# Kernel tuning notes

Measured on AMD Instinct MI355X. Metric: run time of the kernel, lower is better.

Reference implementation:

```python
import jax, jax.numpy as jnp
import numpy as np

N_NODES = 100000


def _gcn_norm(edge_index, n):
    # PyG GCNConv: add self-loops, symmetric normalization D^-1/2 (A+I) D^-1/2
    loops = jnp.arange(n, dtype=edge_index.dtype)
    src = jnp.concatenate([edge_index[0], loops])
    dst = jnp.concatenate([edge_index[1], loops])
    deg = jax.ops.segment_sum(jnp.ones_like(dst, dtype=jnp.float32), dst, num_segments=n)
    dis = jnp.where(deg > 0, jax.lax.rsqrt(jnp.maximum(deg, 1.0)), 0.0)
    norm = dis[src] * dis[dst]  # [E + n]
    return src, dst, norm


def _gcn_layer(h, W, b, src, dst, norm, n):
    h = h @ W                              # dense projection [n, out]
    msg = h[src] * norm[:, None]           # gather + scale   [E+n, out]
    agg = jax.ops.segment_sum(msg, dst, num_segments=n)  # scatter-add
    return agg + b


def setup_inputs() -> dict:
    key = jax.random.key(0)
    ks = jax.random.split(key, 8)
    n, f, h, d, e = N_NODES, 256, 128, 64, 1600000
    x = jax.random.normal(ks[0], (n, f), dtype=jnp.float32)
    edge_index = jax.random.randint(ks[1], (2, e), 0, n, dtype=jnp.int64)
    s1 = 1.0 / np.sqrt(f)
    s2 = 1.0 / np.sqrt(h)
    return {
        "x": x,
        "edge_index": edge_index,
        "W1": jax.random.normal(ks[2], (f, h), dtype=jnp.float32) * s1,
        "b1": jnp.zeros((h,), dtype=jnp.float32),
        "Wmu": jax.random.normal(ks[3], (h, d), dtype=jnp.float32) * s2,
        "bmu": jnp.zeros((d,), dtype=jnp.float32),
        "Wvar": jax.random.normal(ks[4], (h, d), dtype=jnp.float32) * s2,
        "bvar": jnp.zeros((d,), dtype=jnp.float32),
    }


def reference(x, edge_index, W1, b1, Wmu, bmu, Wvar, bvar):
    n = x.shape[0]
    src, dst, norm = _gcn_norm(edge_index, n)
    h = jax.nn.relu(_gcn_layer(x, W1, b1, src, dst, norm, n))
    mu = _gcn_layer(h, Wmu, bmu, src, dst, norm, n)
    sigma = _gcn_layer(h, Wvar, bvar, src, dst, norm, n)
    return mu, sigma
```

## Files before the change

kernel.cpp:

```cpp
#include <hip/hip_runtime.h>


#define HID 128
#define DOUT 64
#define NB_SHIFT 8
#define CHUNK 8192
#define MAXNB 400

typedef _Float16 half_t;
typedef half_t f16x4 __attribute__((ext_vector_type(4)));
typedef half_t f16x8 __attribute__((ext_vector_type(8)));
typedef float  f32x4 __attribute__((ext_vector_type(4)));


__global__ __launch_bounds__(256) void bincount_kernel(const int* __restrict__ dst,
                                                       int* __restrict__ counts,
                                                       int E, int nblocks, int NB) {
    __shared__ int hist[MAXNB];
    const int b = blockIdx.x;
    for (int t = threadIdx.x; t < NB; t += 256) hist[t] = 0;
    __syncthreads();
    const int beg = b * CHUNK;
    const int end = min(E, beg + CHUNK);
    for (int e = beg + threadIdx.x; e < end; e += 256)
        atomicAdd(&hist[dst[e] >> NB_SHIFT], 1);
    __syncthreads();
    for (int t = threadIdx.x; t < NB; t += 256)
        counts[t * nblocks + b] = hist[t];
}

__global__ __launch_bounds__(256) void scan1_kernel(const int* __restrict__ in,
                                                    int* __restrict__ out,
                                                    int* __restrict__ bsum, int n) {
    __shared__ int s[256];
    int b = blockIdx.x, t = threadIdx.x;
    int base = b * 1024 + t * 4;
    int v0 = 0, v1 = 0, v2 = 0, v3 = 0;
    if (base + 0 < n) v0 = in[base + 0];
    if (base + 1 < n) v1 = in[base + 1];
    if (base + 2 < n) v2 = in[base + 2];
    if (base + 3 < n) v3 = in[base + 3];
    int tsum = v0 + v1 + v2 + v3;
    s[t] = tsum;
    __syncthreads();
    for (int off = 1; off < 256; off <<= 1) {
        int x = (t >= off) ? s[t - off] : 0;
        __syncthreads();
        s[t] += x;
        __syncthreads();
    }
    int excl = s[t] - tsum;
    if (base + 0 < n) out[base + 0] = excl;
    if (base + 1 < n) out[base + 1] = excl + v0;
    if (base + 2 < n) out[base + 2] = excl + v0 + v1;
    if (base + 3 < n) out[base + 3] = excl + v0 + v1 + v2;
    if (t == 255) bsum[b] = s[255];
}

__global__ __launch_bounds__(1024) void scan2_kernel(int* __restrict__ bsum, int nb) {
    __shared__ int s[1024];
    int t = threadIdx.x;
    int v = (t < nb) ? bsum[t] : 0;
    s[t] = v;
    __syncthreads();
    for (int off = 1; off < 1024; off <<= 1) {
        int x = (t >= off) ? s[t - off] : 0;
        __syncthreads();
        s[t] += x;
        __syncthreads();
    }
    if (t < nb) bsum[t] = s[t] - v;
}

__global__ void scan3_kernel(int* __restrict__ out, const int* __restrict__ bsum, int n) {
    int i = blockIdx.x * blockDim.x + threadIdx.x;
    if (i < n) out[i] += bsum[i >> 10];
}

__global__ __launch_bounds__(1024) void binscatter_kernel(const int* __restrict__ src,
                                                          const int* __restrict__ dst,
                                                          const int* __restrict__ offsets,
                                                          int2* __restrict__ binned,
                                                          int E, int nblocks, int NB) {
    __shared__ int  lhist[1024];
    __shared__ int  lbase[1024];
    __shared__ int  cur[1024];
    __shared__ int  goff[MAXNB];
    __shared__ int2 staged[CHUNK];
    const int b = blockIdx.x, t = threadIdx.x;
    const int beg = b * CHUNK;
    const int end = min(E, beg + CHUNK);
    const int ne  = end - beg;

    lhist[t] = 0;
    for (int k = t; k < NB; k += 1024) goff[k] = offsets[k * nblocks + b];
    __syncthreads();

    int2 regs[8];
    #pragma unroll
    for (int j = 0; j < 8; j++) {
        int e = beg + t + j * 1024;
        if (e < end) {
            regs[j] = make_int2(src[e], dst[e]);
            atomicAdd(&lhist[regs[j].y >> NB_SHIFT], 1);
        }
    }
    __syncthreads();

    int hv = lhist[t];
    for (int off = 1; off < 1024; off <<= 1) {
        int x = (t >= off) ? lhist[t - off] : 0;
        __syncthreads();
        lhist[t] += x;
        __syncthreads();
    }
    lbase[t] = lhist[t] - hv;
    cur[t]   = lhist[t] - hv;
    __syncthreads();

    #pragma unroll
    for (int j = 0; j < 8; j++) {
        int e = beg + t + j * 1024;
        if (e < end) {
            int pos = atomicAdd(&cur[regs[j].y >> NB_SHIFT], 1);
            staged[pos] = regs[j];
        }
    }
    __syncthreads();

    #pragma unroll
    for (int j = 0; j < 8; j++) {
        int tt = t + j * 1024;
        if (tt < ne) {
            int2 sd = staged[tt];
            int bkt = sd.y >> NB_SHIFT;
            binned[goff[bkt] + (tt - lbase[bkt])] = sd;
        }
    }
}

__global__ __launch_bounds__(256) void csrbuild_kernel(const int2* __restrict__ binned,
                                                       const int* __restrict__ offsets,
                                                       int* __restrict__ rowptr_end,
                                                       int* __restrict__ colA,
                                                       float* __restrict__ dis,
                                                       int E, int nblocks, int NB, int n) {
    __shared__ int deg[256];
    __shared__ int sc[256];
    __shared__ int cur[256];
    const int b = blockIdx.x;
    const int t = threadIdx.x;
    const int base = offsets[b * nblocks];
    const int bend = (b + 1 < NB) ? offsets[(b + 1) * nblocks] : E;

    deg[t] = 0;
    __syncthreads();
    for (int e = base + t; e < bend; e += 256)
        atomicAdd(&deg[binned[e].y & 255], 1);
    __syncthreads();

    int v = deg[t];
    sc[t] = v;
    __syncthreads();
    for (int off = 1; off < 256; off <<= 1) {
        int x = (t >= off) ? sc[t - off] : 0;
        __syncthreads();
        sc[t] += x;
        __syncthreads();
    }
    int incl = sc[t];
    int node = (b << NB_SHIFT) + t;
    if (node < n) {
        rowptr_end[node] = base + incl;
        dis[node] = rsqrtf((float)v + 1.0f);
    }
    cur[t] = base + incl - v;
    __syncthreads();

    for (int e = base + t; e < bend; e += 256) {
        int2 sd = binned[e];
        int pos = atomicAdd(&cur[sd.y & 255], 1);
        colA[pos] = sd.x;
    }
}

__global__ void w1t_kernel(const float* __restrict__ W1, half_t* __restrict__ W1T) {
    int i = blockIdx.x * blockDim.x + threadIdx.x;
    int k = i >> 7, nn = i & 127;
    W1T[nn * 256 + k] = (half_t)W1[i];
}
__global__ void wcatt_kernel(const float* __restrict__ Wmu, const float* __restrict__ Wvar,
                             half_t* __restrict__ WcatT) {
    int i = blockIdx.x * blockDim.x + threadIdx.x;
    int k = i >> 7, nn = i & 127;
    float v = (nn < DOUT) ? Wmu[k * DOUT + nn] : Wvar[k * DOUT + (nn - DOUT)];
    WcatT[nn * 128 + k] = (half_t)v;
}

__global__ __launch_bounds__(256) void gemm1_mfma(const float* __restrict__ A,
                                                  const half_t* __restrict__ BT,
                                                  const float* __restrict__ dis,
                                                  half_t* __restrict__ C, int M) {
    __shared__ half_t As[64][72];
    __shared__ half_t Bs[128][72];
    const int tid = threadIdx.x;
    const int block_row = blockIdx.x * 64;
    const int wave = tid >> 6, lane = tid & 63;
    const int wm = (wave & 1) * 32, wn = (wave >> 1) * 64;
    const int l16 = lane & 15, quad = lane >> 4;

    f32x4 acc[2][4] = {};
    float4 pa[4];
    f16x8  pb[4];

    #pragma unroll
    for (int i = 0; i < 4; i++) {
        int idx = tid + i * 256;
        int r = idx >> 4, c = idx & 15;
        int row = block_row + r; row = row < M ? row : M - 1;
        pa[i] = ((const float4*)(A + (size_t)row * 256))[c];
    }
    #pragma unroll
    for (int i = 0; i < 4; i++) {
        int idx = tid + i * 256;
        int nr = idx >> 3, kc = idx & 7;
        pb[i] = *(const f16x8*)(BT + (size_t)nr * 256 + kc * 8);
    }

    for (int k0 = 0; k0 < 256; k0 += 64) {
        #pragma unroll
        for (int i = 0; i < 4; i++) {
            int idx = tid + i * 256;
            int r = idx >> 4, c = idx & 15;
            f16x4 hv = { (half_t)pa[i].x, (half_t)pa[i].y, (half_t)pa[i].z, (half_t)pa[i].w };
            *(f16x4*)(&As[r][c * 4]) = hv;
        }
        #pragma unroll
        for (int i = 0; i < 4; i++) {
            int idx = tid + i * 256;
            int nr = idx >> 3, kc = idx & 7;
            *(f16x8*)(&Bs[nr][kc * 8]) = pb[i];
        }
        __syncthreads();

        if (k0 < 192) {
            #pragma unroll
            for (int i = 0; i < 4; i++) {
                int idx = tid + i * 256;
                int r = idx >> 4, c = idx & 15;
                int row = block_row + r; row = row < M ? row : M - 1;
                pa[i] = ((const float4*)(A + (size_t)row * 256 + k0 + 64))[c];
            }
            #pragma unroll
            for (int i = 0; i < 4; i++) {
                int idx = tid + i * 256;
                int nr = idx >> 3, kc = idx & 7;
                pb[i] = *(const f16x8*)(BT + (size_t)nr * 256 + k0 + 64 + kc * 8);
            }
        }

        #pragma unroll
        for (int ks = 0; ks < 2; ks++) {
            f16x8 af[2], bf[4];
            #pragma unroll
            for (int mt = 0; mt < 2; mt++)
                af[mt] = *(const f16x8*)(&As[wm + mt * 16 + l16][ks * 32 + quad * 8]);
            #pragma unroll
            for (int nt = 0; nt < 4; nt++)
                bf[nt] = *(const f16x8*)(&Bs[wn + nt * 16 + l16][ks * 32 + quad * 8]);
            #pragma unroll
            for (int mt = 0; mt < 2; mt++)
                #pragma unroll
                for (int nt = 0; nt < 4; nt++)
                    acc[mt][nt] = __builtin_amdgcn_mfma_f32_16x16x32_f16(af[mt], bf[nt], acc[mt][nt], 0, 0, 0);
        }
        __syncthreads();
    }

    #pragma unroll
    for (int mt = 0; mt < 2; mt++) {
        #pragma unroll
        for (int r = 0; r < 4; r++) {
            int row = block_row + wm + mt * 16 + quad * 4 + r;
            if (row < M) {
                float d = dis[row];
                #pragma unroll
                for (int nt = 0; nt < 4; nt++) {
                    int col = wn + nt * 16 + l16;
                    C[(size_t)row * 128 + col] = (half_t)(acc[mt][nt][r] * d);
                }
            }
        }
    }
}

__global__ __launch_bounds__(256) void gemm2_mfma(const half_t* __restrict__ A,
                                                  const half_t* __restrict__ BT,
                                                  const float* __restrict__ bmu,
                                                  const float* __restrict__ bvar,
                                                  float* __restrict__ out_mu,
                                                  float* __restrict__ out_sig, int M) {
    __shared__ half_t As[64][72];
    __shared__ half_t Bs[128][72];
    const int tid = threadIdx.x;
    const int block_row = blockIdx.x * 64;
    const int wave = tid >> 6, lane = tid & 63;
    const int wm = (wave & 1) * 32, wn = (wave >> 1) * 64;
    const int l16 = lane & 15, quad = lane >> 4;

    f32x4 acc[2][4] = {};
    f16x8 pa[2], pb[4];

    #pragma unroll
    for (int i = 0; i < 2; i++) {
        int idx = tid + i * 256;
        int r = idx >> 3, kc = idx & 7;
        int row = block_row + r; row = row < M ? row : M - 1;
        pa[i] = *(const f16x8*)(A + (size_t)row * 128 + kc * 8);
    }
    #pragma unroll
    for (int i = 0; i < 4; i++) {
        int idx = tid + i * 256;
        int nr = idx >> 3, kc = idx & 7;
        pb[i] = *(const f16x8*)(BT + (size_t)nr * 128 + kc * 8);
    }

    for (int k0 = 0; k0 < 128; k0 += 64) {
        #pragma unroll
        for (int i = 0; i < 2; i++) {
            int idx = tid + i * 256;
            int r = idx >> 3, kc = idx & 7;
            *(f16x8*)(&As[r][kc * 8]) = pa[i];
        }
        #pragma unroll
        for (int i = 0; i < 4; i++) {
            int idx = tid + i * 256;
            int nr = idx >> 3, kc = idx & 7;
            *(f16x8*)(&Bs[nr][kc * 8]) = pb[i];
        }
        __syncthreads();

        if (k0 < 64) {
            #pragma unroll
            for (int i = 0; i < 2; i++) {
                int idx = tid + i * 256;
                int r = idx >> 3, kc = idx & 7;
                int row = block_row + r; row = row < M ? row : M - 1;
                pa[i] = *(const f16x8*)(A + (size_t)row * 128 + 64 + kc * 8);
            }
            #pragma unroll
            for (int i = 0; i < 4; i++) {
                int idx = tid + i * 256;
                int nr = idx >> 3, kc = idx & 7;
                pb[i] = *(const f16x8*)(BT + (size_t)nr * 128 + 64 + kc * 8);
            }
        }

        #pragma unroll
        for (int ks = 0; ks < 2; ks++) {
            f16x8 af[2], bf[4];
            #pragma unroll
            for (int mt = 0; mt < 2; mt++)
                af[mt] = *(const f16x8*)(&As[wm + mt * 16 + l16][ks * 32 + quad * 8]);
            #pragma unroll
            for (int nt = 0; nt < 4; nt++)
                bf[nt] = *(const f16x8*)(&Bs[wn + nt * 16 + l16][ks * 32 + quad * 8]);
            #pragma unroll
            for (int mt = 0; mt < 2; mt++)
                #pragma unroll
                for (int nt = 0; nt < 4; nt++)
                    acc[mt][nt] = __builtin_amdgcn_mfma_f32_16x16x32_f16(af[mt], bf[nt], acc[mt][nt], 0, 0, 0);
        }
        __syncthreads();
    }

    float bias[4];
    int cols[4];
    #pragma unroll
    for (int nt = 0; nt < 4; nt++) {
        int col = wn + nt * 16 + l16;
        cols[nt] = col;
        bias[nt] = (col < DOUT) ? bmu[col] : bvar[col - DOUT];
    }

    #pragma unroll
    for (int mt = 0; mt < 2; mt++) {
        #pragma unroll
        for (int r = 0; r < 4; r++) {
            int row = block_row + wm + mt * 16 + quad * 4 + r;
            if (row < M) {
                #pragma unroll
                for (int nt = 0; nt < 4; nt++) {
                    int col = cols[nt];
                    float v = acc[mt][nt][r] + bias[nt];
                    if (col < DOUT) out_mu[(size_t)row * DOUT + col] = v;
                    else            out_sig[(size_t)row * DOUT + (col - DOUT)] = v;
                }
            }
        }
    }
}

__device__ __forceinline__ void acc_mix(float& a0, float& a1, float& a2, float& a3,
                                        f16x4 v, float fl) {
    union { f16x4 h; int i[2]; } u; u.h = v;
    asm("v_fma_mix_f32 %0, %1, %2, %0 op_sel_hi:[1,0,0]"
        : "+v"(a0) : "v"(u.i[0]), "v"(fl));
    asm("v_fma_mix_f32 %0, %1, %2, %0 op_sel:[1,0,0] op_sel_hi:[1,0,0]"
        : "+v"(a1) : "v"(u.i[0]), "v"(fl));
    asm("v_fma_mix_f32 %0, %1, %2, %0 op_sel_hi:[1,0,0]"
        : "+v"(a2) : "v"(u.i[1]), "v"(fl));
    asm("v_fma_mix_f32 %0, %1, %2, %0 op_sel:[1,0,0] op_sel_hi:[1,0,0]"
        : "+v"(a3) : "v"(u.i[1]), "v"(fl));
}

template <bool LAYER1>
__global__ __launch_bounds__(256) void agg_kernel(const int* __restrict__ rowptr_end,
                                                  const int* __restrict__ col,
                                                  const float* __restrict__ dis,
                                                  const half_t* __restrict__ hin,
                                                  half_t* __restrict__ hout,
                                                  const float* __restrict__ bias, int n) {
    int node = blockIdx.x * 8 + (threadIdx.x >> 5);
    if (node >= n) return;
    int lane = threadIdx.x & 31;
    int beg = (node == 0) ? 0 : rowptr_end[node - 1];
    int end = rowptr_end[node];
    const f16x4* hv = (const f16x4*)hin;

    float one = 1.0f;
    float ax = 0.f, ay = 0.f, az = 0.f, aw = 0.f;
    acc_mix(ax, ay, az, aw, hv[(size_t)node * 32 + lane], one);

    int deg = end - beg;
    if (deg > 0) {
        const int last = end - 1;
        int c[8];
        #pragma unroll
        for (int j = 0; j < 8; j++) c[j] = col[min(beg + j, last)];

        int ng = (deg + 7) >> 3;
        int e = beg;
        for (int g = 0; g < ng; g++) {
            f16x4 v[8];
            #pragma unroll
            for (int j = 0; j < 8; j++) v[j] = hv[(size_t)c[j] * 32 + lane];

            int enext = e + 8;
            if (g + 1 < ng) {
                #pragma unroll
                for (int j = 0; j < 8; j++) c[j] = col[min(enext + j, last)];
                #pragma unroll
                for (int j = 0; j < 8; j++) acc_mix(ax, ay, az, aw, v[j], one);
            } else {
                int rem = end - e;
                #pragma unroll
                for (int j = 0; j < 8; j++) {
                    float fl = (j < rem) ? 1.0f : 0.0f;
                    acc_mix(ax, ay, az, aw, v[j], fl);
                }
            }
            e = enext;
        }
    }

    float di = dis[node];
    if (LAYER1) {
        const float4 b = ((const float4*)bias)[lane];
        ax = ax * di + b.x; ay = ay * di + b.y; az = az * di + b.z; aw = aw * di + b.w;
        ax = (ax > 0.f ? ax : 0.f) * di;
        ay = (ay > 0.f ? ay : 0.f) * di;
        az = (az > 0.f ? az : 0.f) * di;
        aw = (aw > 0.f ? aw : 0.f) * di;
    } else {
        ax *= di; ay *= di; az *= di; aw *= di;
    }
    f16x4 o = { (half_t)ax, (half_t)ay, (half_t)az, (half_t)aw };
    ((f16x4*)hout)[(size_t)node * 32 + lane] = o;
}

extern "C" void kernel_launch(void* const* d_in, const int* in_sizes, int n_in,
                              void* d_out, int out_size, void* d_ws, size_t ws_size,
                              hipStream_t stream) {
    const float* x    = (const float*)d_in[0];
    const int*   ei   = (const int*)d_in[1];
    const float* W1   = (const float*)d_in[2];
    const float* b1   = (const float*)d_in[3];
    const float* Wmu  = (const float*)d_in[4];
    const float* bmu  = (const float*)d_in[5];
    const float* Wvar = (const float*)d_in[6];
    const float* bvar = (const float*)d_in[7];

    const int n = in_sizes[0] / 256;
    const int E = in_sizes[1] / 2;
    const int* src = ei;
    const int* dst = ei + E;

    const int NB      = (n + 255) >> NB_SHIFT;
    const int nblocks = (E + CHUNK - 1) / CHUNK;
    const int flat    = NB * nblocks;
    const int nb_scan = (flat + 1023) / 1024;

    char* ws = (char*)d_ws;
    size_t off = 0;
    auto alloc = [&](size_t bytes) { void* p = ws + off; off = (off + bytes + 255) & ~(size_t)255; return p; };
    float*  dis     = (float*) alloc((size_t)n * 4);
    int*    rowptr  = (int*)   alloc((size_t)n * 4);
    int*    counts  = (int*)   alloc((size_t)flat * 4);
    int*    offsets = (int*)   alloc((size_t)flat * 4);
    int*    bsum    = (int*)   alloc((size_t)nb_scan * 4 + 256);
    int2*   binned  = (int2*)  alloc((size_t)E * 8);
    int*    col     = (int*)   alloc((size_t)E * 4);
    half_t* W1T     = (half_t*)alloc((size_t)256 * HID * 2);
    half_t* WcatT   = (half_t*)alloc((size_t)HID * HID * 2);
    half_t* hs      = (half_t*)alloc((size_t)n * HID * 2);
    half_t* h1s     = (half_t*)alloc((size_t)n * HID * 2);
    half_t* agg2    = hs;

    float* out_mu  = (float*)d_out;
    float* out_sig = (float*)d_out + (size_t)n * DOUT;

    bincount_kernel<<<nblocks, 256, 0, stream>>>(dst, counts, E, nblocks, NB);
    scan1_kernel<<<nb_scan, 256, 0, stream>>>(counts, offsets, bsum, flat);
    scan2_kernel<<<1, 1024, 0, stream>>>(bsum, nb_scan);
    scan3_kernel<<<(flat + 255) / 256, 256, 0, stream>>>(offsets, bsum, flat);
    binscatter_kernel<<<nblocks, 1024, 0, stream>>>(src, dst, offsets, binned, E, nblocks, NB);
    csrbuild_kernel<<<NB, 256, 0, stream>>>(binned, offsets, rowptr, col, dis, E, nblocks, NB, n);

    w1t_kernel<<<(256 * HID) / 256, 256, 0, stream>>>(W1, W1T);
    wcatt_kernel<<<(HID * HID) / 256, 256, 0, stream>>>(Wmu, Wvar, WcatT);

    gemm1_mfma<<<(n + 63) / 64, 256, 0, stream>>>(x, W1T, dis, hs, n);
    agg_kernel<true><<<(n + 7) / 8, 256, 0, stream>>>(rowptr, col, dis, hs, h1s, b1, n);
    agg_kernel<false><<<(n + 7) / 8, 256, 0, stream>>>(rowptr, col, dis, h1s, agg2, nullptr, n);
    gemm2_mfma<<<(n + 63) / 64, 256, 0, stream>>>(agg2, WcatT, bmu, bvar, out_mu, out_sig, n);
}
```

Baseline: 217.6 us.

## Store hidden features in column-chunked layout and split aggregation by feature chunk

The hidden feature matrices now use a chunk-major layout of 8 chunks of 16 halves per node, written by gemm1 and read by gemm2 and the aggregation kernels. The aggregation grid is multiplied by 8 so each block handles one feature chunk, with 8 edge slots per node processed in parallel and reduced through warp shuffles. The aim is to make each chunk's working set (n×16 halves) fit in cache, so the random neighbour gathers hit cache more often. In exchange, the col array is read 8 times over, shuffle reductions are added, and each gather is only 8 bytes wide.

```diff
diff --git a/kernel.cpp b/kernel.cpp
--- a/kernel.cpp
+++ b/kernel.cpp
@@ -286,8 +286,8 @@
                 float d = dis[row];
                 #pragma unroll
                 for (int nt = 0; nt < 4; nt++) {
-                    int col = wn + nt * 16 + l16;
-                    C[(size_t)row * 128 + col] = (half_t)(acc[mt][nt][r] * d);
+                    int cchunk = (wn >> 4) + nt;
+                    C[((size_t)cchunk * M + row) * 16 + l16] = (half_t)(acc[mt][nt][r] * d);
                 }
             }
         }
@@ -316,7 +316,7 @@
         int idx = tid + i * 256;
         int r = idx >> 3, kc = idx & 7;
         int row = block_row + r; row = row < M ? row : M - 1;
-        pa[i] = *(const f16x8*)(A + (size_t)row * 128 + kc * 8);
+        pa[i] = *(const f16x8*)(A + ((size_t)(kc >> 1) * M + row) * 16 + (kc & 1) * 8);
     }
     #pragma unroll
     for (int i = 0; i < 4; i++) {
@@ -346,7 +346,7 @@
                 int idx = tid + i * 256;
                 int r = idx >> 3, kc = idx & 7;
                 int row = block_row + r; row = row < M ? row : M - 1;
-                pa[i] = *(const f16x8*)(A + (size_t)row * 128 + 64 + kc * 8);
+                pa[i] = *(const f16x8*)(A + ((size_t)(4 + (kc >> 1)) * M + row) * 16 + (kc & 1) * 8);
             }
             #pragma unroll
             for (int i = 0; i < 4; i++) {
@@ -421,62 +421,63 @@
                                                   const half_t* __restrict__ hin,
                                                   half_t* __restrict__ hout,
                                                   const float* __restrict__ bias, int n) {
-    int node = blockIdx.x * 8 + (threadIdx.x >> 5);
+    const int chunk = blockIdx.x & 7;
+    const int node  = (blockIdx.x >> 3) * 8 + (threadIdx.x >> 5);
     if (node >= n) return;
-    int lane = threadIdx.x & 31;
-    int beg = (node == 0) ? 0 : rowptr_end[node - 1];
-    int end = rowptr_end[node];
-    const f16x4* hv = (const f16x4*)hin;
-
-    float one = 1.0f;
+    const int lane32 = threadIdx.x & 31;
+    const int fq   = lane32 & 3;
+    const int slot = lane32 >> 2;
+
+    const f16x4* hc = (const f16x4*)(hin + (size_t)chunk * n * 16);
+
+    int beg = (node == 0) ? 0 : __builtin_nontemporal_load(&rowptr_end[node - 1]);
+    int end = __builtin_nontemporal_load(&rowptr_end[node]);
+
     float ax = 0.f, ay = 0.f, az = 0.f, aw = 0.f;
-    acc_mix(ax, ay, az, aw, hv[(size_t)node * 32 + lane], one);
+    {
+        f16x4 sv = hc[node * 4 + fq];
+        float fl = (slot == 0) ? 1.0f : 0.0f;
+        acc_mix(ax, ay, az, aw, sv, fl);
+    }
 
     int deg = end - beg;
     if (deg > 0) {
         const int last = end - 1;
-        int c[8];
-        #pragma unroll
-        for (int j = 0; j < 8; j++) c[j] = col[min(beg + j, last)];
-
+        int e = beg + slot;
+        int c = __builtin_nontemporal_load(&col[min(e, last)]);
         int ng = (deg + 7) >> 3;
-        int e = beg;
         for (int g = 0; g < ng; g++) {
-            f16x4 v[8];
-            #pragma unroll
-            for (int j = 0; j < 8; j++) v[j] = hv[(size_t)c[j] * 32 + lane];
-
-            int enext = e + 8;
-            if (g + 1 < ng) {
-                #pragma unroll
-                for (int j = 0; j < 8; j++) c[j] = col[min(enext + j, last)];
-                #pragma unroll
-                for (int j = 0; j < 8; j++) acc_mix(ax, ay, az, aw, v[j], one);
-            } else {
-                int rem = end - e;
-                #pragma unroll
-                for (int j = 0; j < 8; j++) {
-                    float fl = (j < rem) ? 1.0f : 0.0f;
-                    acc_mix(ax, ay, az, aw, v[j], fl);
-                }
-            }
-            e = enext;
-        }
-    }
-
-    float di = dis[node];
-    if (LAYER1) {
-        const float4 b = ((const float4*)bias)[lane];
-        ax = ax * di + b.x; ay = ay * di + b.y; az = az * di + b.z; aw = aw * di + b.w;
-        ax = (ax > 0.f ? ax : 0.f) * di;
-        ay = (ay > 0.f ? ay : 0.f) * di;
-        az = (az > 0.f ? az : 0.f) * di;
-        aw = (aw > 0.f ? aw : 0.f) * di;
-    } else {
-        ax *= di; ay *= di; az *= di; aw *= di;
-    }
-    f16x4 o = { (half_t)ax, (half_t)ay, (half_t)az, (half_t)aw };
-    ((f16x4*)hout)[(size_t)node * 32 + lane] = o;
+            f16x4 v = hc[c * 4 + fq];
+            int en = e + 8;
+            c = __builtin_nontemporal_load(&col[min(en, last)]);
+            float fl = (e <= last) ? 1.0f : 0.0f;
+            acc_mix(ax, ay, az, aw, v, fl);
+            e = en;
+        }
+    }
+
+    ax += __shfl_xor(ax, 4);  ay += __shfl_xor(ay, 4);
+    az += __shfl_xor(az, 4);  aw += __shfl_xor(aw, 4);
+    ax += __shfl_xor(ax, 8);  ay += __shfl_xor(ay, 8);
+    az += __shfl_xor(az, 8);  aw += __shfl_xor(aw, 8);
+    ax += __shfl_xor(ax, 16); ay += __shfl_xor(ay, 16);
+    az += __shfl_xor(az, 16); aw += __shfl_xor(aw, 16);
+
+    if (slot == 0) {
+        float di = dis[node];
+        if (LAYER1) {
+            const float4 b = ((const float4*)bias)[chunk * 4 + fq];
+            ax = ax * di + b.x; ay = ay * di + b.y; az = az * di + b.z; aw = aw * di + b.w;
+            ax = (ax > 0.f ? ax : 0.f) * di;
+            ay = (ay > 0.f ? ay : 0.f) * di;
+            az = (az > 0.f ? az : 0.f) * di;
+            aw = (aw > 0.f ? aw : 0.f) * di;
+        } else {
+            ax *= di; ay *= di; az *= di; aw *= di;
+        }
+        f16x4 o = { (half_t)ax, (half_t)ay, (half_t)az, (half_t)aw };
+        ((f16x4*)(hout + (size_t)chunk * n * 16))[node * 4 + fq] = o;
+    }
 }
 
 extern "C" void kernel_launch(void* const* d_in, const int* in_sizes, int n_in,
@@ -530,8 +531,9 @@
     w1t_kernel<<<(256 * HID) / 256, 256, 0, stream>>>(W1, W1T);
     wcatt_kernel<<<(HID * HID) / 256, 256, 0, stream>>>(Wmu, Wvar, WcatT);
 
+    const int aggGrid = ((n + 7) / 8) * 8;
     gemm1_mfma<<<(n + 63) / 64, 256, 0, stream>>>(x, W1T, dis, hs, n);
-    agg_kernel<true><<<(n + 7) / 8, 256, 0, stream>>>(rowptr, col, dis, hs, h1s, b1, n);
-    agg_kernel<false><<<(n + 7) / 8, 256, 0, stream>>>(rowptr, col, dis, h1s, agg2, nullptr, n);
+    agg_kernel<true><<<aggGrid, 256, 0, stream>>>(rowptr, col, dis, hs, h1s, b1, n);
+    agg_kernel<false><<<aggGrid, 256, 0, stream>>>(rowptr, col, dis, h1s, agg2, nullptr, n);
     gemm2_mfma<<<(n + 63) / 64, 256, 0, stream>>>(agg2, WcatT, bmu, bvar, out_mu, out_sig, n);
 }
```

Result: slower. 461.2 us (+111.9%).

## Store hidden features in column-chunked layout to shrink gather working set per pass

Applied to the files above, without the earlier changes.

Hidden feature matrices are now stored as 8 column chunks of 16 halves per node, so each aggregation block handles one chunk for 64 nodes with 4 lanes per node. Blocks of consecutive blockIdx share a node range but cover different chunks, so each pass gathers from a 3.2MB slice that fits in cache, aiming to raise L2 hit rates for random neighbour gathers. The trade-off is that CSR indices are re-read 8 times, which is why those loads are marked nontemporal, and each gathered row is only 32 bytes. GEMM1 output and GEMM2 input addressing are adapted to the new layout.

```diff
diff --git a/kernel.cpp b/kernel.cpp
--- a/kernel.cpp
+++ b/kernel.cpp
@@ -286,8 +286,8 @@
                 float d = dis[row];
                 #pragma unroll
                 for (int nt = 0; nt < 4; nt++) {
-                    int col = wn + nt * 16 + l16;
-                    C[(size_t)row * 128 + col] = (half_t)(acc[mt][nt][r] * d);
+                    int cchunk = (wn >> 4) + nt;
+                    C[((size_t)cchunk * M + row) * 16 + l16] = (half_t)(acc[mt][nt][r] * d);
                 }
             }
         }
@@ -316,7 +316,7 @@
         int idx = tid + i * 256;
         int r = idx >> 3, kc = idx & 7;
         int row = block_row + r; row = row < M ? row : M - 1;
-        pa[i] = *(const f16x8*)(A + (size_t)row * 128 + kc * 8);
+        pa[i] = *(const f16x8*)(A + ((size_t)(kc >> 1) * M + row) * 16 + (kc & 1) * 8);
     }
     #pragma unroll
     for (int i = 0; i < 4; i++) {
@@ -346,7 +346,7 @@
                 int idx = tid + i * 256;
                 int r = idx >> 3, kc = idx & 7;
                 int row = block_row + r; row = row < M ? row : M - 1;
-                pa[i] = *(const f16x8*)(A + (size_t)row * 128 + 64 + kc * 8);
+                pa[i] = *(const f16x8*)(A + ((size_t)(4 + (kc >> 1)) * M + row) * 16 + (kc & 1) * 8);
             }
             #pragma unroll
             for (int i = 0; i < 4; i++) {
@@ -421,35 +421,40 @@
                                                   const half_t* __restrict__ hin,
                                                   half_t* __restrict__ hout,
                                                   const float* __restrict__ bias, int n) {
-    int node = blockIdx.x * 8 + (threadIdx.x >> 5);
+    const int chunk = blockIdx.x & 7;
+    const int node  = (blockIdx.x >> 3) * 64 + (threadIdx.x >> 2);
     if (node >= n) return;
-    int lane = threadIdx.x & 31;
+    const int fq = threadIdx.x & 3;
+
+    const f16x4* hc = (const f16x4*)(hin + (size_t)chunk * n * 16);
+
     int beg = (node == 0) ? 0 : rowptr_end[node - 1];
     int end = rowptr_end[node];
-    const f16x4* hv = (const f16x4*)hin;
 
     float one = 1.0f;
     float ax = 0.f, ay = 0.f, az = 0.f, aw = 0.f;
-    acc_mix(ax, ay, az, aw, hv[(size_t)node * 32 + lane], one);
+    acc_mix(ax, ay, az, aw, hc[node * 4 + fq], one);
 
     int deg = end - beg;
     if (deg > 0) {
         const int last = end - 1;
         int c[8];
         #pragma unroll
-        for (int j = 0; j < 8; j++) c[j] = col[min(beg + j, last)];
+        for (int j = 0; j < 8; j++)
+            c[j] = __builtin_nontemporal_load(&col[min(beg + j, last)]);
 
         int ng = (deg + 7) >> 3;
         int e = beg;
         for (int g = 0; g < ng; g++) {
             f16x4 v[8];
             #pragma unroll
-            for (int j = 0; j < 8; j++) v[j] = hv[(size_t)c[j] * 32 + lane];
+            for (int j = 0; j < 8; j++) v[j] = hc[c[j] * 4 + fq];
 
             int enext = e + 8;
             if (g + 1 < ng) {
                 #pragma unroll
-                for (int j = 0; j < 8; j++) c[j] = col[min(enext + j, last)];
+                for (int j = 0; j < 8; j++)
+                    c[j] = __builtin_nontemporal_load(&col[min(enext + j, last)]);
                 #pragma unroll
                 for (int j = 0; j < 8; j++) acc_mix(ax, ay, az, aw, v[j], one);
             } else {
@@ -466,7 +471,7 @@
 
     float di = dis[node];
     if (LAYER1) {
-        const float4 b = ((const float4*)bias)[lane];
+        const float4 b = ((const float4*)bias)[chunk * 4 + fq];
         ax = ax * di + b.x; ay = ay * di + b.y; az = az * di + b.z; aw = aw * di + b.w;
         ax = (ax > 0.f ? ax : 0.f) * di;
         ay = (ay > 0.f ? ay : 0.f) * di;
@@ -476,7 +481,7 @@
         ax *= di; ay *= di; az *= di; aw *= di;
     }
     f16x4 o = { (half_t)ax, (half_t)ay, (half_t)az, (half_t)aw };
-    ((f16x4*)hout)[(size_t)node * 32 + lane] = o;
+    ((f16x4*)(hout + (size_t)chunk * n * 16))[node * 4 + fq] = o;
 }
 
 extern "C" void kernel_launch(void* const* d_in, const int* in_sizes, int n_in,
@@ -530,8 +535,9 @@
     w1t_kernel<<<(256 * HID) / 256, 256, 0, stream>>>(W1, W1T);
     wcatt_kernel<<<(HID * HID) / 256, 256, 0, stream>>>(Wmu, Wvar, WcatT);
 
+    const int aggGrid = ((n + 63) / 64) * 8;
     gemm1_mfma<<<(n + 63) / 64, 256, 0, stream>>>(x, W1T, dis, hs, n);
-    agg_kernel<true><<<(n + 7) / 8, 256, 0, stream>>>(rowptr, col, dis, hs, h1s, b1, n);
-    agg_kernel<false><<<(n + 7) / 8, 256, 0, stream>>>(rowptr, col, dis, h1s, agg2, nullptr, n);
+    agg_kernel<true><<<aggGrid, 256, 0, stream>>>(rowptr, col, dis, hs, h1s, b1, n);
+    agg_kernel<false><<<aggGrid, 256, 0, stream>>>(rowptr, col, dis, h1s, agg2, nullptr, n);
     gemm2_mfma<<<(n + 63) / 64, 256, 0, stream>>>(agg2, WcatT, bmu, bvar, out_mu, out_sig, n);
 }
```

After: 391.4 us. +79.8%, slower.
